# Kernel optimization log

Hardware: AMD Instinct MI355X
Metric: run time of the kernel (lower is better)

The kernel has to match this reference:

```python
import jax, jax.numpy as jnp
import numpy as np

N_NODES = 40000
N_EDGES = 400000
N_GRAPHS = 256
F_IN = 128
COND = 100
HEADS = 32
DIMS = [90, 45, 15, 5]
EPS = 1e-5


def setup_inputs() -> dict:
    key = jax.random.key(0)
    ks = iter(jax.random.split(key, 64))
    inp = {}
    inp["x"] = jax.random.normal(next(ks), (N_NODES, F_IN), dtype=jnp.float32)
    inp["edge_index"] = jax.random.randint(next(ks), (2, N_EDGES), 0, N_NODES, dtype=jnp.int32)
    inp["batch"] = jnp.sort(jax.random.randint(next(ks), (N_NODES,), 0, N_GRAPHS, dtype=jnp.int32))
    inp["conditional_features"] = jax.random.normal(next(ks), (COND,), dtype=jnp.float32)
    # GATConv params: W [in, H*C], a_src/a_dst [H, C], bias [C] (concat=False -> out is C)
    dims_in = [F_IN] + DIMS[:-1]
    for i, (ci, co) in enumerate(zip(dims_in, DIMS), start=1):
        sw = 1.0 / np.sqrt(ci)
        inp[f"W{i}"] = jax.random.normal(next(ks), (ci, HEADS * co), dtype=jnp.float32) * sw
        inp[f"as{i}"] = jax.random.normal(next(ks), (HEADS, co), dtype=jnp.float32) * (1.0 / np.sqrt(co))
        inp[f"ad{i}"] = jax.random.normal(next(ks), (HEADS, co), dtype=jnp.float32) * (1.0 / np.sqrt(co))
        inp[f"b{i}"] = jnp.zeros((co,), dtype=jnp.float32)
    # BatchNorm affine params (init gamma=1, beta=0) for sizes F_IN,90,45,15,5
    for i, c in enumerate([F_IN] + DIMS, start=1):
        inp[f"g{i}"] = jnp.ones((c,), dtype=jnp.float32)
        inp[f"be{i}"] = jnp.zeros((c,), dtype=jnp.float32)
    inp["fcW"] = jax.random.normal(next(ks), (DIMS[-1] + COND, 1), dtype=jnp.float32) * (1.0 / np.sqrt(DIMS[-1] + COND))
    inp["fcb"] = jnp.zeros((1,), dtype=jnp.float32)
    return inp


def _bn(x, g, b):
    # training-mode BatchNorm1d: batch statistics (biased var), eps=1e-5
    mu = x.mean(0)
    var = x.var(0)
    return g * (x - mu) * jax.lax.rsqrt(var + EPS) + b


def _gat(x, W, a_s, a_d, b, src, dst, n):
    H, C = a_s.shape
    h = (x @ W).reshape(n, H, C)                      # [N,H,C]
    s_src = jnp.einsum("nhc,hc->nh", h, a_s)
    s_dst = jnp.einsum("nhc,hc->nh", h, a_d)
    logit = jax.nn.leaky_relu(s_src[src] + s_dst[dst], 0.2)  # [E,H]
    m = jax.ops.segment_max(logit, dst, num_segments=n)
    e = jnp.exp(logit - m[dst])
    denom = jax.ops.segment_sum(e, dst, num_segments=n)
    alpha = e / denom[dst]                            # per-dst softmax, [E,H]
    out = jnp.zeros((n, C), dtype=x.dtype)
    for hi in range(H):  # fixed small loop over heads keeps peak memory at [E,C]
        out = out + jax.ops.segment_sum(alpha[:, hi, None] * h[src, hi, :], dst, num_segments=n)
    return out / H + b   # concat=False -> mean over heads, then bias


def reference(x, edge_index, batch, conditional_features,
              W1, as1, ad1, b1, W2, as2, ad2, b2, W3, as3, ad3, b3, W4, as4, ad4, b4,
              g1, be1, g2, be2, g3, be3, g4, be4, g5, be5, fcW, fcb):
    n = x.shape[0]
    loop = jnp.arange(n, dtype=edge_index.dtype)      # PyG GATConv adds self-loops by default
    src = jnp.concatenate([edge_index[0], loop])
    dst = jnp.concatenate([edge_index[1], loop])

    h = _bn(x, g1, be1)
    h = jax.nn.leaky_relu(_gat(h, W1, as1, ad1, b1, src, dst, n), 0.01)
    h = _bn(h, g2, be2)
    h = jax.nn.leaky_relu(_gat(h, W2, as2, ad2, b2, src, dst, n), 0.01)
    h = _bn(h, g3, be3)
    h = jax.nn.leaky_relu(_gat(h, W3, as3, ad3, b3, src, dst, n), 0.01)
    h = _bn(h, g4, be4)
    h = jax.nn.leaky_relu(_gat(h, W4, as4, ad4, b4, src, dst, n), 0.01)
    # dropout is identity in eval mode

    counts = jax.ops.segment_sum(jnp.ones((n,), dtype=h.dtype), batch, num_segments=N_GRAPHS)
    pooled = jax.ops.segment_sum(h, batch, num_segments=N_GRAPHS) / jnp.maximum(counts, 1.0)[:, None]
    z = jnp.concatenate([pooled, jnp.broadcast_to(conditional_features, (N_GRAPHS, COND))], axis=1)
    return jax.nn.sigmoid(z @ fcW + fcb).reshape(-1, 1)
```

## Files before the change

kernel.cpp:

```cpp
#include <hip/hip_runtime.h>
#include <hip/hip_bf16.h>

constexpr int NN = 40000;
constexpr int NE = 400000;
constexpr int NSLAB = 20000;
constexpr int MPAD = 20096;
constexpr int SCB = 256;
constexpr int SCHUNK = (NN + SCB - 1) / SCB;
constexpr int NPB = 512;

__device__ __forceinline__ unsigned short f2bf(float f) {
    unsigned int u = __float_as_uint(f);
    unsigned int r = (u + 0x7FFFu + ((u >> 16) & 1u)) >> 16;
    return (unsigned short)r;
}

__device__ __forceinline__ unsigned int cvt_pk_bf16(float a, float b) {
    unsigned int r;
    asm("v_cvt_pk_bf16_f32 %0, %1, %2" : "=v"(r) : "v"(a), "v"(b));
    return r;
}

__device__ __forceinline__ void load_lds16(const unsigned short* g, unsigned short* l) {
    __builtin_amdgcn_global_load_lds(
        (const __attribute__((address_space(1))) unsigned int*)(g),
        (__attribute__((address_space(3))) unsigned int*)(l), 16, 0, 0);
}

typedef __attribute__((ext_vector_type(8))) short bf16x8;
typedef __attribute__((ext_vector_type(4))) float f32x4;
typedef __attribute__((ext_vector_type(2))) float floatx2;

__global__ void bn_partial(const float* __restrict__ x, int N, int C,
                           float* __restrict__ partial) {
    int ch = threadIdx.x;
    if (ch >= C) return;
    float s = 0.f, sq = 0.f;
    for (int n = blockIdx.x; n < N; n += gridDim.x) {
        float v = x[(size_t)n * C + ch];
        s += v; sq += v * v;
    }
    partial[(size_t)blockIdx.x * 2 * C + ch]     = s;
    partial[(size_t)blockIdx.x * 2 * C + C + ch] = sq;
}

template <int CIN, int CP>
__global__ __launch_bounds__(256) void bn_apply_f(const float* __restrict__ x,
                                                  const float* __restrict__ partial,
                                                  const float* __restrict__ g,
                                                  const float* __restrict__ be,
                                                  float* __restrict__ scale_g,
                                                  float* __restrict__ shift_g,
                                                  unsigned short* __restrict__ xbn) {
    __shared__ float hs[2][128], hq[2][128];
    __shared__ float sc_l[CP], sh_l[CP];
    const int tid = threadIdx.x;
    const int half = tid >> 7, ch = tid & 127;
    if (ch < CIN) {
        float s = 0.f, sq = 0.f;
        for (int b = half * (NPB / 2); b < (half + 1) * (NPB / 2); ++b) {
            s  += partial[(size_t)b * 2 * CIN + ch];
            sq += partial[(size_t)b * 2 * CIN + CIN + ch];
        }
        hs[half][ch] = s; hq[half][ch] = sq;
    }
    __syncthreads();
    if (tid < CP) {
        float sc = 0.f, sh = 0.f;
        if (tid < CIN) {
            float s  = hs[0][tid] + hs[1][tid];
            float sq = hq[0][tid] + hq[1][tid];
            float mean = s / (float)NN;
            float var  = sq / (float)NN - mean * mean;
            float inv  = rsqrtf(var + 1e-5f);
            sc = g[tid] * inv;
            sh = be[tid] - mean * sc;
            if (blockIdx.x == 0) { scale_g[tid] = sc; shift_g[tid] = sh; }
        }
        sc_l[tid] = sc; sh_l[tid] = sh;
    }
    __syncthreads();
    const int total = NN * (CP / 2);
    for (int idx = blockIdx.x * 256 + tid; idx < total; idx += 256 * gridDim.x) {
        int n = idx / (CP / 2), c2 = idx % (CP / 2);
        int c = 2 * c2;
        float v0 = 0.f, v1 = 0.f;
        if (c < CIN)     v0 = sc_l[c] * x[(size_t)n * CIN + c] + sh_l[c];
        if (c + 1 < CIN) v1 = sc_l[c + 1] * x[(size_t)n * CIN + c + 1] + sh_l[c + 1];
        reinterpret_cast<unsigned int*>(xbn)[idx] = cvt_pk_bf16(v0, v1);
    }
}

struct PrepLayer {
    const float* W; const float* as_; const float* ad_;
    float* Wf; unsigned short* Wft; unsigned short* Wt;
    int CIN, CP, COUT, NP, bbase;
};
struct PrepArgs { PrepLayer L[4]; int nb; };

__global__ void prep_all(PrepArgs A) {
    int bid = blockIdx.x;
    int li = 0;
#pragma unroll
    for (int i = 1; i < 4; ++i)
        if (bid >= A.L[i].bbase) li = i;
    const PrepLayer& P = A.L[li];
    const int CIN = P.CIN, CP = P.CP, COUT = P.COUT;
    int b = bid - P.bbase;
    int tid = threadIdx.x;
    if (b < CP) {
        int cin = b;
        if (tid < 64) {
            int j = tid, h = j & 31;
            float s = 0.f;
            if (cin < CIN) {
                const float* a = (j < 32) ? P.as_ : P.ad_;
                const float* wrow = P.W + (size_t)cin * 32 * COUT + (size_t)h * COUT;
                const float* arow = a + (size_t)h * COUT;
                for (int c = 0; c < COUT; ++c) s += wrow[c] * arow[c];
            }
            P.Wf[cin * 64 + j] = s;
            P.Wft[j * CP + cin] = f2bf(s);
        }
    } else {
        int c = b - CP;
        for (int kk = tid; kk < 32 * CP; kk += blockDim.x) {
            int h = kk / CP, k = kk % CP;
            float v = 0.f;
            if (k < CIN && c < COUT)
                v = P.W[(size_t)k * (32 * COUT) + h * COUT + c] * (1.f / 32.f);
            P.Wt[(size_t)c * (32 * CP) + kk] = f2bf(v);
        }
    }
}

template <int CPK>
__global__ __launch_bounds__(256) void gemm_s(const unsigned short* __restrict__ xbn,
                                              const unsigned short* __restrict__ Wft,
                                              float* __restrict__ Sbuf) {
    constexpr int NC = CPK / 32;
    __shared__ unsigned short Ab[64 * 32];
    __shared__ unsigned short Bb[64 * 32];
    const int m0 = blockIdx.x * 64;
    const int tid = threadIdx.x;
    const int wv = tid >> 6, lane = tid & 63;
    const int mm = lane & 15, quad = lane >> 4;
    f32x4 acc[4];
#pragma unroll
    for (int t = 0; t < 4; ++t) acc[t] = f32x4{0.f, 0.f, 0.f, 0.f};

    for (int c = 0; c < NC; ++c) {
        int row = tid >> 2, gc = tid & 3;
        load_lds16(xbn + (size_t)(m0 + row) * CPK + c * 32 + gc * 8, Ab + (size_t)tid * 8);
        load_lds16(Wft + (size_t)row * CPK + c * 32 + gc * 8, Bb + (size_t)tid * 8);
        asm volatile("s_waitcnt vmcnt(0)" ::: "memory");
        __syncthreads();
        bf16x8 a = *reinterpret_cast<const bf16x8*>(&Ab[(wv * 16 + mm) * 32 + quad * 8]);
#pragma unroll
        for (int t = 0; t < 4; ++t) {
            bf16x8 b = *reinterpret_cast<const bf16x8*>(&Bb[(t * 16 + mm) * 32 + quad * 8]);
            acc[t] = __builtin_amdgcn_mfma_f32_16x16x32_bf16(a, b, acc[t], 0, 0, 0);
        }
        __syncthreads();
    }
    int rbase = m0 + wv * 16 + quad * 4;
#pragma unroll
    for (int t = 0; t < 4; ++t)
#pragma unroll
        for (int r = 0; r < 4; ++r)
            Sbuf[(size_t)(rbase + r) * 64 + t * 16 + mm] = acc[t][r];
}

__global__ __launch_bounds__(256) void gemm_bn(const float* __restrict__ X,
                                               const float* __restrict__ W,
                                               const float* __restrict__ scale,
                                               const float* __restrict__ shift,
                                               int Cin, int HC, float* __restrict__ OUT) {
    __shared__ float As[8][64];
    __shared__ float Bs[8][64];
    int tid = threadIdx.x;
    int n0 = blockIdx.y * 64;
    int j0 = blockIdx.x * 64;
    int tr = tid >> 4, tc = tid & 15;
    float acc[4][4] = {};
    for (int k0 = 0; k0 < Cin; k0 += 8) {
        int idx = tid;
#pragma unroll
        for (int it = 0; it < 2; ++it, idx += 256) {
            int row = idx >> 3, kk = idx & 7;
            int k = k0 + kk;
            float v = 0.f;
            if (k < Cin) v = scale[k] * X[(size_t)(n0 + row) * Cin + k] + shift[k];
            As[kk][row] = v;
        }
        int idx2 = tid;
#pragma unroll
        for (int it = 0; it < 2; ++it, idx2 += 256) {
            int col = idx2 & 63, kr = idx2 >> 6;
            int k = k0 + kr, j = j0 + col;
            float v = 0.f;
            if (k < Cin && j < HC) v = W[(size_t)k * HC + j];
            Bs[kr][col] = v;
        }
        __syncthreads();
#pragma unroll
        for (int kk = 0; kk < 8; ++kk) {
            float a[4], b[4];
#pragma unroll
            for (int i = 0; i < 4; ++i) a[i] = As[kk][tr * 4 + i];
#pragma unroll
            for (int j = 0; j < 4; ++j) b[j] = Bs[kk][tc * 4 + j];
#pragma unroll
            for (int i = 0; i < 4; ++i)
#pragma unroll
                for (int j = 0; j < 4; ++j) acc[i][j] += a[i] * b[j];
        }
        __syncthreads();
    }
#pragma unroll
    for (int i = 0; i < 4; ++i) {
        int row = n0 + tr * 4 + i;
#pragma unroll
        for (int j = 0; j < 4; ++j) {
            int col = j0 + tc * 4 + j;
            if (col < HC) OUT[(size_t)row * HC + col] = acc[i][j];
        }
    }
}

__global__ void count_kernel(const int* __restrict__ dst, int* __restrict__ deg) {
    int e = blockIdx.x * blockDim.x + threadIdx.x;
    if (e < NE) atomicAdd(&deg[dst[e]], 1);
}
__global__ void scan_pass1(const int* __restrict__ deg, int* __restrict__ bsum) {
    __shared__ int red[256];
    int b = blockIdx.x, t = threadIdx.x;
    int lo = b * SCHUNK, hi = min(lo + SCHUNK, NN);
    int s = 0;
    for (int i = lo + t; i < hi; i += 256) s += deg[i] + 1;
    red[t] = s;
    __syncthreads();
    for (int off = 128; off > 0; off >>= 1) {
        if (t < off) red[t] += red[t + off];
        __syncthreads();
    }
    if (t == 0) bsum[b] = red[0];
}
__global__ void scan_pass2(const int* __restrict__ bsum, int* __restrict__ boff,
                           int* __restrict__ rowptr) {
    __shared__ int lds[256];
    int t = threadIdx.x;
    int v0 = bsum[t];
    lds[t] = v0;
    __syncthreads();
    for (int off = 1; off < 256; off <<= 1) {
        int v = (t >= off) ? lds[t - off] : 0;
        __syncthreads();
        lds[t] += v;
        __syncthreads();
    }
    boff[t] = lds[t] - v0;
    if (t == 255) rowptr[NN] = lds[255];
}
__global__ void scan_pass3(const int* __restrict__ deg, const int* __restrict__ boff,
                           int* __restrict__ rowptr, int* __restrict__ cursor) {
    __shared__ int lds[256];
    int b = blockIdx.x, t = threadIdx.x;
    int i = b * SCHUNK + t;
    int d = (t < SCHUNK && i < NN) ? (deg[i] + 1) : 0;
    lds[t] = d;
    __syncthreads();
    for (int off = 1; off < 256; off <<= 1) {
        int v = (t >= off) ? lds[t - off] : 0;
        __syncthreads();
        lds[t] += v;
        __syncthreads();
    }
    if (t < SCHUNK && i < NN) {
        int excl = lds[t] - d + boff[b];
        rowptr[i] = excl;
        cursor[i] = excl;
    }
}
__global__ void scatter_all(const int* __restrict__ src, const int* __restrict__ dst,
                            int* __restrict__ cursor, int* __restrict__ colsrc) {
    int e = blockIdx.x * blockDim.x + threadIdx.x;
    if (e < NE) {
        int pos = atomicAdd(&cursor[dst[e]], 1);
        colsrc[pos] = src[e];
    } else if (e < NE + NN) {
        int n = e - NE;
        int pos = atomicAdd(&cursor[n], 1);
        colsrc[pos] = n;
    }
}

template <int CIN, int CP>
__global__ __launch_bounds__(256) void agg_x(const unsigned short* __restrict__ xbn,
                                             const float* __restrict__ S,
                                             const int* __restrict__ rowptr,
                                             const int* __restrict__ colsrc,
                                             int n0, unsigned short* __restrict__ z) {
    constexpr int BS = 256, CH = 16, J = CP / 8;
    constexpr bool V4 = (J % 4 == 0);
    constexpr int NACC = V4 ? (J / 4) : (J / 2);
    constexpr int LIT = CH * 32 / 256;
    __shared__ __align__(16) float x_lds[CH * CP];
    __shared__ float w_lds[CH * 32];
    __shared__ int cs_lds[CH];
    __shared__ float red_m[8][32];
    __shared__ float red_s[8][32];

    int n = n0 + blockIdx.x;
    int tid = threadIdx.x;
    int start = rowptr[n], end = rowptr[n + 1];
    const int h = tid & 31, g = tid >> 5;
    const int cbase = g * J;
    const float sd = S[(size_t)n * 64 + 32 + h];

    float m_reg = -INFINITY, d_reg = 0.f;
    f32x4 acc4[V4 ? NACC : 1];
    floatx2 acc2[V4 ? 1 : NACC];
    if constexpr (V4) {
#pragma unroll
        for (int j = 0; j < NACC; ++j) acc4[j] = f32x4{0.f, 0.f, 0.f, 0.f};
    } else {
#pragma unroll
        for (int j = 0; j < NACC; ++j) acc2[j] = floatx2{0.f, 0.f};
    }

    for (int chunk = start; chunk < end; chunk += CH) {
        int ce = min(CH, end - chunk);
        int ce32 = ce * 32;
        if (tid < CH && tid < ce) cs_lds[tid] = colsrc[chunk + tid];
        __syncthreads();

        float lreg[LIT];
        float pmx = -INFINITY;
#pragma unroll
        for (int p = 0; p < LIT; ++p) {
            int idx = p * 256 + tid;
            lreg[p] = -INFINITY;
            if (idx < ce32) {
                int e = idx >> 5;
                float l = S[(size_t)cs_lds[e] * 64 + h] + sd;
                l = l > 0.f ? l : 0.2f * l;
                lreg[p] = l;
                pmx = fmaxf(pmx, l);
            }
        }
        red_m[g][h] = pmx;
        for (int idx = tid; idx < ce * (CP / 4); idx += BS) {
            int e = idx / (CP / 4), c4 = idx % (CP / 4);
            uint2 u = reinterpret_cast<const uint2*>(xbn)[(size_t)cs_lds[e] * (CP / 4) + c4];
            f32x4 t;
            t[0] = __uint_as_float(u.x << 16);
            t[1] = __uint_as_float(u.x & 0xFFFF0000u);
            t[2] = __uint_as_float(u.y << 16);
            t[3] = __uint_as_float(u.y & 0xFFFF0000u);
            *reinterpret_cast<f32x4*>(&x_lds[e * CP + 4 * c4]) = t;
        }
        __syncthreads();

        float cm = red_m[0][h];
#pragma unroll
        for (int s2 = 1; s2 < 8; ++s2) cm = fmaxf(cm, red_m[s2][h]);
        float newm = fmaxf(m_reg, cm);
        float r = (m_reg == -INFINITY) ? 0.f : __expf(m_reg - newm);
        m_reg = newm;

        float ps = 0.f;
#pragma unroll
        for (int p = 0; p < LIT; ++p) {
            int idx = p * 256 + tid;
            if (idx < ce32) {
                float v = __expf(lreg[p] - m_reg);
                w_lds[idx] = v;
                ps += v;
            }
        }
        red_s[g][h] = ps;
        __syncthreads();

        float ss = red_s[0][h];
#pragma unroll
        for (int s2 = 1; s2 < 8; ++s2) ss += red_s[s2][h];
        d_reg = d_reg * r + ss;

        if constexpr (V4) {
            f32x4 rr4 = {r, r, r, r};
#pragma unroll
            for (int j = 0; j < NACC; ++j) acc4[j] *= rr4;
            for (int e = 0; e < ce; ++e) {
                float w = w_lds[e * 32 + h];
                f32x4 w4 = {w, w, w, w};
                const f32x4* xv = reinterpret_cast<const f32x4*>(&x_lds[e * CP + cbase]);
#pragma unroll
                for (int j = 0; j < NACC; ++j) acc4[j] += w4 * xv[j];
            }
        } else {
            floatx2 rr2 = {r, r};
#pragma unroll
            for (int j = 0; j < NACC; ++j) acc2[j] *= rr2;
            for (int e = 0; e < ce; ++e) {
                float w = w_lds[e * 32 + h];
                floatx2 w2 = {w, w};
                const floatx2* xv = reinterpret_cast<const floatx2*>(&x_lds[e * CP + cbase]);
#pragma unroll
                for (int j = 0; j < NACC; ++j) acc2[j] += w2 * xv[j];
            }
        }
    }

    float dinv = 1.f / d_reg;
    if constexpr (V4) {
        uint2* zp = reinterpret_cast<uint2*>(
            z + (size_t)(n - n0) * (32 * CP) + h * CP + cbase);
#pragma unroll
        for (int j = 0; j < NACC; ++j) {
            uint2 t;
            t.x = cvt_pk_bf16(acc4[j][0] * dinv, acc4[j][1] * dinv);
            t.y = cvt_pk_bf16(acc4[j][2] * dinv, acc4[j][3] * dinv);
            zp[j] = t;
        }
    } else {
        unsigned int* zp = reinterpret_cast<unsigned int*>(
            z + (size_t)(n - n0) * (32 * CP) + h * CP + cbase);
#pragma unroll
        for (int j = 0; j < NACC; ++j)
            zp[j] = cvt_pk_bf16(acc2[j][0] * dinv, acc2[j][1] * dinv);
    }
}

template <int NT, int KP, int KS, bool FB>
__global__ __launch_bounds__(256) void gemm_z_t(const unsigned short* __restrict__ z,
                                                const unsigned short* __restrict__ Wt,
                                                float* __restrict__ obuf,
                                                const float* __restrict__ bias,
                                                int n0, int COUT) {
    constexpr int NP = NT * 16;
    constexpr int KSEG = KP / KS;
    constexpr int NC = KSEG / 64;
    constexpr int MT = 64;
    __shared__ unsigned short Abuf[2][MT * 64];
    __shared__ unsigned short Bbuf[2][NP * 64];

    const int m0 = blockIdx.x * MT;
    const int kbeg = blockIdx.y * KSEG;
    const int tid = threadIdx.x;
    const int wv = tid >> 6;
    const int lane = tid & 63;
    const int mm = lane & 15, quad = lane >> 4;

    auto stage = [&](int buf, int kk) {
#pragma unroll
        for (int it = 0; it < 2; ++it) {
            int gi = it * 256 + tid;
            int row = gi >> 3, gc = gi & 7;
            int srow = m0 + row;
            if (srow > NSLAB - 1) srow = NSLAB - 1;
            const unsigned short* src = z + (size_t)srow * KP + kk + gc * 8;
            unsigned short* dst = &Abuf[buf][(size_t)(it * 256 + wv * 64) * 8];
            load_lds16(src, dst);
        }
#pragma unroll
        for (int it = 0; it < (NP * 8 + 255) / 256; ++it) {
            int gi = it * 256 + tid;
            if (gi < NP * 8) {
                int row = gi >> 3, gc = gi & 7;
                const unsigned short* src = Wt + (size_t)row * KP + kk + gc * 8;
                unsigned short* dst = &Bbuf[buf][(size_t)(it * 256 + wv * 64) * 8];
                load_lds16(src, dst);
            }
        }
    };

    f32x4 acc[NT];
#pragma unroll
    for (int t = 0; t < NT; ++t) acc[t] = f32x4{0.f, 0.f, 0.f, 0.f};

    stage(0, kbeg);
    for (int c = 0; c < NC; ++c) {
        asm volatile("s_waitcnt vmcnt(0)" ::: "memory");
        __syncthreads();
        int cur = c & 1;
        if (c + 1 < NC) stage(cur ^ 1, kbeg + (c + 1) * 64);
        const unsigned short* Ab = Abuf[cur];
        const unsigned short* Bb = Bbuf[cur];
#pragma unroll
        for (int hh = 0; hh < 2; ++hh) {
            bf16x8 a0 = *reinterpret_cast<const bf16x8*>(&Ab[(wv * 16 + mm) * 64 + hh * 32 + quad * 8]);
#pragma unroll
            for (int t = 0; t < NT; ++t) {
                bf16x8 b = *reinterpret_cast<const bf16x8*>(&Bb[(t * 16 + mm) * 64 + hh * 32 + quad * 8]);
                acc[t] = __builtin_amdgcn_mfma_f32_16x16x32_bf16(a0, b, acc[t], 0, 0, 0);
            }
        }
        __syncthreads();
    }

    int row0 = quad * 4;
    if constexpr (FB) {
#pragma unroll
        for (int t = 0; t < NT; ++t) {
            int cc = t * 16 + mm;
#pragma unroll
            for (int r = 0; r < 4; ++r) {
                int m = m0 + wv * 16 + row0 + r;
                if (m < NSLAB && cc < COUT) {
                    float v = acc[t][r] + bias[cc];
                    v = v > 0.f ? v : 0.01f * v;
                    obuf[(size_t)(n0 + m) * COUT + cc] = v;
                }
            }
        }
    } else {
        float* pb = obuf + (size_t)blockIdx.y * MPAD * NP;
#pragma unroll
        for (int t = 0; t < NT; ++t) {
            int cc = t * 16 + mm;
#pragma unroll
            for (int r = 0; r < 4; ++r) {
                int m = m0 + wv * 16 + row0 + r;
                pb[(size_t)m * NP + cc] = acc[t][r];
            }
        }
    }
}

__global__ void reduce_parts(const float* __restrict__ pbuf, int KS, int NPAD, int COUT,
                             const float* __restrict__ bias, int n0,
                             float* __restrict__ xout) {
    int idx = blockIdx.x * blockDim.x + threadIdx.x;
    if (idx >= NSLAB * NPAD) return;
    int m = idx / NPAD, c = idx % NPAD;
    if (c >= COUT) return;
    float s = 0.f;
    for (int p = 0; p < KS; ++p) s += pbuf[(size_t)p * MPAD * NPAD + (size_t)m * NPAD + c];
    float v = s + bias[c];
    v = v > 0.f ? v : 0.01f * v;
    xout[(size_t)(n0 + m) * COUT + c] = v;
}

__global__ __launch_bounds__(64) void pool_head(const float* __restrict__ x4,
                                                const int* __restrict__ batch,
                                                const float* __restrict__ cond,
                                                const float* __restrict__ fcW,
                                                const float* __restrict__ fcb,
                                                float* __restrict__ out) {
    int g = blockIdx.x;
    int lane = threadIdx.x;
    int lo = 0, hi = NN;
    while (lo < hi) { int mid = (lo + hi) >> 1; if (batch[mid] < g) lo = mid + 1; else hi = mid; }
    int lo2 = lo, hi2 = NN;
    while (lo2 < hi2) { int mid = (lo2 + hi2) >> 1; if (batch[mid] < g + 1) lo2 = mid + 1; else hi2 = mid; }
    int beg = lo, end = lo2;

    float s[5] = {0.f, 0.f, 0.f, 0.f, 0.f};
    for (int n = beg + lane; n < end; n += 64) {
#pragma unroll
        for (int c = 0; c < 5; ++c) s[c] += x4[(size_t)n * 5 + c];
    }
    float cz = 0.f;
    if (lane < 100) cz = cond[lane] * fcW[5 + lane];
    if (lane + 64 < 100) cz += cond[lane + 64] * fcW[5 + lane + 64];
#pragma unroll
    for (int off = 32; off > 0; off >>= 1) {
#pragma unroll
        for (int c = 0; c < 5; ++c) s[c] += __shfl_down(s[c], off, 64);
        cz += __shfl_down(cz, off, 64);
    }
    if (lane == 0) {
        float cnt = fmaxf((float)(end - beg), 1.f);
        float zv = fcb[0] + cz;
#pragma unroll
        for (int c = 0; c < 5; ++c) zv += (s[c] / cnt) * fcW[c];
        out[g] = 1.f / (1.f + __expf(-zv));
    }
}

struct LayerBufs {
    float* partial; float* scale; float* shift;
    unsigned short* xbn; unsigned short* zbuf;
    float* Sbuf; float* pbuf; const int* rowptr; const int* colsrc;
};

template <int CIN, int CP, int COUT, int NP, int NT, int KS>
static void run_layer(const float* xin, const float* Wf, const unsigned short* Wft,
                      const unsigned short* Wt,
                      const float* Bv, const float* G, const float* Be,
                      float* xout, const LayerBufs& B, hipStream_t stream) {
    constexpr int KP = 32 * CP;
    constexpr int NPAD = NT * 16;
    bn_partial<<<NPB, 128, 0, stream>>>(xin, NN, CIN, B.partial);
    bn_apply_f<CIN, CP><<<512, 256, 0, stream>>>(xin, B.partial, G, Be,
                                                 B.scale, B.shift, B.xbn);
    if constexpr (CP >= 64) {
        gemm_s<CP><<<NN / 64, 256, 0, stream>>>(B.xbn, Wft, B.Sbuf);
    } else {
        gemm_bn<<<dim3(1, NN / 64), 256, 0, stream>>>(xin, Wf, B.scale, B.shift, CIN, 64, B.Sbuf);
    }
    for (int s = 0; s < 2; ++s) {
        int n0 = s * NSLAB;
        agg_x<CIN, CP><<<NSLAB, 256, 0, stream>>>(B.xbn, B.Sbuf, B.rowptr, B.colsrc, n0, B.zbuf);
        if constexpr (KS > 1) {
            gemm_z_t<NT, KP, KS, false><<<dim3(MPAD / 64, KS), 256, 0, stream>>>(
                B.zbuf, Wt, B.pbuf, nullptr, n0, COUT);
            reduce_parts<<<(NSLAB * NPAD + 255) / 256, 256, 0, stream>>>(
                B.pbuf, KS, NPAD, COUT, Bv, n0, xout);
        } else {
            gemm_z_t<NT, KP, 1, true><<<dim3(MPAD / 64, 1), 256, 0, stream>>>(
                B.zbuf, Wt, xout, Bv, n0, COUT);
        }
    }
}

extern "C" void kernel_launch(void* const* d_in, const int* in_sizes, int n_in,
                              void* d_out, int out_size, void* d_ws, size_t ws_size,
                              hipStream_t stream) {
    (void)in_sizes; (void)n_in; (void)out_size;
    const float* x     = (const float*)d_in[0];
    const int*   ei    = (const int*)d_in[1];
    const int*   batch = (const int*)d_in[2];
    const float* cond  = (const float*)d_in[3];
    const float* W[4]  = {(const float*)d_in[4],  (const float*)d_in[8],
                          (const float*)d_in[12], (const float*)d_in[16]};
    const float* Asp[4] = {(const float*)d_in[5],  (const float*)d_in[9],
                           (const float*)d_in[13], (const float*)d_in[17]};
    const float* Adp[4] = {(const float*)d_in[6],  (const float*)d_in[10],
                           (const float*)d_in[14], (const float*)d_in[18]};
    const float* Bv[4]  = {(const float*)d_in[7],  (const float*)d_in[11],
                           (const float*)d_in[15], (const float*)d_in[19]};
    const float* G[4]   = {(const float*)d_in[20], (const float*)d_in[22],
                           (const float*)d_in[24], (const float*)d_in[26]};
    const float* Be[4]  = {(const float*)d_in[21], (const float*)d_in[23],
                           (const float*)d_in[25], (const float*)d_in[27]};
    const float* fcW = (const float*)d_in[30];
    const float* fcb = (const float*)d_in[31];
    float* out = (float*)d_out;

    char* base = (char*)d_ws;
    size_t off = 0;
    auto alloc = [&](size_t b) {
        size_t o = off;
        off += (b + 255) & ~(size_t)255;
        return (void*)(base + o);
    };
    unsigned short* zbuf = (unsigned short*)alloc((size_t)NSLAB * 4096 * 2);
    unsigned short* xbn  = (unsigned short*)alloc((size_t)NN * 128 * 2);
    float* pbuf    = (float*)alloc((size_t)4 * MPAD * 96 * 4);
    float* xbuf    = (float*)alloc((size_t)NN * 90 * 4);
    float* Sbuf    = (float*)alloc((size_t)NN * 64 * 4);
    float* partial = (float*)alloc((size_t)NPB * 2 * 128 * 4);
    float* scale   = (float*)alloc(128 * 4);
    float* shift   = (float*)alloc(128 * 4);
    const int CPs[4]  = {128, 96, 48, 16};
    const int NPs[4]  = {96, 48, 16, 16};
    const int CINs[4] = {128, 90, 45, 15};
    const int COUTs[4] = {90, 45, 15, 5};
    float* Wf_a[4]; unsigned short* Wft_a[4]; unsigned short* Wt_a[4];
    for (int i = 0; i < 4; ++i) {
        Wf_a[i]  = (float*)alloc((size_t)CPs[i] * 64 * 4);
        Wft_a[i] = (unsigned short*)alloc((size_t)64 * CPs[i] * 2);
        Wt_a[i]  = (unsigned short*)alloc((size_t)NPs[i] * 32 * CPs[i] * 2);
    }
    int* deg     = (int*)alloc((size_t)NN * 4);
    int* rowptr  = (int*)alloc((size_t)(NN + 1) * 4);
    int* cursor  = (int*)alloc((size_t)NN * 4);
    int* colsrc  = (int*)alloc((size_t)(NE + NN) * 4);
    int* bsum    = (int*)alloc((size_t)SCB * 4);
    int* boff    = (int*)alloc((size_t)SCB * 4);
    if (off > ws_size) return;

    const int* srcp = ei;
    const int* dstp = ei + NE;

    PrepArgs PA;
    int bb = 0;
    for (int i = 0; i < 4; ++i) {
        PA.L[i] = PrepLayer{W[i], Asp[i], Adp[i], Wf_a[i], Wft_a[i], Wt_a[i],
                            CINs[i], CPs[i], COUTs[i], NPs[i], bb};
        bb += CPs[i] + NPs[i];
    }
    PA.nb = bb;
    prep_all<<<bb, 256, 0, stream>>>(PA);

    hipMemsetAsync(deg, 0, (size_t)NN * 4, stream);
    count_kernel<<<(NE + 255) / 256, 256, 0, stream>>>(dstp, deg);
    scan_pass1<<<SCB, 256, 0, stream>>>(deg, bsum);
    scan_pass2<<<1, 256, 0, stream>>>(bsum, boff, rowptr);
    scan_pass3<<<SCB, 256, 0, stream>>>(deg, boff, rowptr, cursor);
    scatter_all<<<(NE + NN + 255) / 256, 256, 0, stream>>>(srcp, dstp, cursor, colsrc);

    LayerBufs B{partial, scale, shift, xbn, zbuf, Sbuf, pbuf, rowptr, colsrc};

    run_layer<128, 128, 90, 96, 6, 4>(x,    Wf_a[0], Wft_a[0], Wt_a[0], Bv[0], G[0], Be[0], xbuf, B, stream);
    run_layer< 90,  96, 45, 48, 3, 3>(xbuf, Wf_a[1], Wft_a[1], Wt_a[1], Bv[1], G[1], Be[1], xbuf, B, stream);
    run_layer< 45,  48, 15, 16, 1, 1>(xbuf, Wf_a[2], Wft_a[2], Wt_a[2], Bv[2], G[2], Be[2], xbuf, B, stream);
    run_layer< 15,  16,  5, 16, 1, 1>(xbuf, Wf_a[3], Wft_a[3], Wt_a[3], Bv[3], G[3], Be[3], xbuf, B, stream);

    pool_head<<<256, 64, 0, stream>>>(xbuf, batch, cond, fcW, fcb, out);
}
```

Baseline: 1.018 ms.

## Process two destination nodes per block in GAT aggregation kernel

The aggregation kernel now handles two nodes per 256-thread block, with 128 threads per node and each thread group covering twice as many channels. LDS buffers are duplicated per node, and the grid is halved. The aim is to raise work per thread and amortize block overhead and barriers. In exchange, both nodes loop to the larger degree, so work is imbalanced, and the code assumes CP/4 is a multiple of 4, dropping the float2 path.

```diff
diff --git a/kernel.cpp b/kernel.cpp
--- a/kernel.cpp
+++ b/kernel.cpp
@@ -29,7 +29,6 @@
 
 typedef __attribute__((ext_vector_type(8))) short bf16x8;
 typedef __attribute__((ext_vector_type(4))) float f32x4;
-typedef __attribute__((ext_vector_type(2))) float floatx2;
 
 __global__ void bn_partial(const float* __restrict__ x, int N, int C,
                            float* __restrict__ partial) {
@@ -301,70 +300,74 @@
                                              const int* __restrict__ rowptr,
                                              const int* __restrict__ colsrc,
                                              int n0, unsigned short* __restrict__ z) {
-    constexpr int BS = 256, CH = 16, J = CP / 8;
-    constexpr bool V4 = (J % 4 == 0);
-    constexpr int NACC = V4 ? (J / 4) : (J / 2);
-    constexpr int LIT = CH * 32 / 256;
-    __shared__ __align__(16) float x_lds[CH * CP];
-    __shared__ float w_lds[CH * 32];
-    __shared__ int cs_lds[CH];
-    __shared__ float red_m[8][32];
-    __shared__ float red_s[8][32];
-
-    int n = n0 + blockIdx.x;
-    int tid = threadIdx.x;
-    int start = rowptr[n], end = rowptr[n + 1];
-    const int h = tid & 31, g = tid >> 5;
+    constexpr int CH = 16, J = CP / 4;
+    constexpr int NACC = J / 4;
+    constexpr int LIT = CH * 32 / 128;
+    __shared__ __align__(16) float x_lds[2][CH * CP];
+    __shared__ float w_lds[2][CH * 32];
+    __shared__ int cs_lds[2][CH];
+    __shared__ float red_m[2][4][32];
+    __shared__ float red_s[2][4][32];
+
+    const int tid = threadIdx.x;
+    const int node = tid >> 7;
+    const int tl = tid & 127;
+    const int h = tl & 31, g = tl >> 5;
     const int cbase = g * J;
+    const int nb = n0 + blockIdx.x * 2;
+    const int n = nb + node;
+
+    const int r0 = rowptr[nb], r1 = rowptr[nb + 1], r2 = rowptr[nb + 2];
+    const int start = node ? r1 : r0;
+    const int end   = node ? r2 : r1;
+    const int nch = (max(r1 - r0, r2 - r1) + CH - 1) / CH;
+
     const float sd = S[(size_t)n * 64 + 32 + h];
 
     float m_reg = -INFINITY, d_reg = 0.f;
-    f32x4 acc4[V4 ? NACC : 1];
-    floatx2 acc2[V4 ? 1 : NACC];
-    if constexpr (V4) {
-#pragma unroll
-        for (int j = 0; j < NACC; ++j) acc4[j] = f32x4{0.f, 0.f, 0.f, 0.f};
-    } else {
-#pragma unroll
-        for (int j = 0; j < NACC; ++j) acc2[j] = floatx2{0.f, 0.f};
-    }
-
-    for (int chunk = start; chunk < end; chunk += CH) {
+    f32x4 acc4[NACC];
+#pragma unroll
+    for (int j = 0; j < NACC; ++j) acc4[j] = f32x4{0.f, 0.f, 0.f, 0.f};
+
+    for (int t = 0; t < nch; ++t) {
+        int chunk = start + t * CH;
         int ce = min(CH, end - chunk);
+        if (ce < 0) ce = 0;
         int ce32 = ce * 32;
-        if (tid < CH && tid < ce) cs_lds[tid] = colsrc[chunk + tid];
+        if (tl < CH && tl < ce) cs_lds[node][tl] = colsrc[chunk + tl];
         __syncthreads();
 
         float lreg[LIT];
         float pmx = -INFINITY;
 #pragma unroll
         for (int p = 0; p < LIT; ++p) {
-            int idx = p * 256 + tid;
+            int idx = p * 128 + tl;
             lreg[p] = -INFINITY;
             if (idx < ce32) {
                 int e = idx >> 5;
-                float l = S[(size_t)cs_lds[e] * 64 + h] + sd;
+                float l = S[(size_t)cs_lds[node][e] * 64 + h] + sd;
                 l = l > 0.f ? l : 0.2f * l;
                 lreg[p] = l;
                 pmx = fmaxf(pmx, l);
             }
         }
-        red_m[g][h] = pmx;
-        for (int idx = tid; idx < ce * (CP / 4); idx += BS) {
+        red_m[node][g][h] = pmx;
+        for (int idx = tl; idx < ce * (CP / 4); idx += 128) {
             int e = idx / (CP / 4), c4 = idx % (CP / 4);
-            uint2 u = reinterpret_cast<const uint2*>(xbn)[(size_t)cs_lds[e] * (CP / 4) + c4];
-            f32x4 t;
-            t[0] = __uint_as_float(u.x << 16);
-            t[1] = __uint_as_float(u.x & 0xFFFF0000u);
-            t[2] = __uint_as_float(u.y << 16);
-            t[3] = __uint_as_float(u.y & 0xFFFF0000u);
-            *reinterpret_cast<f32x4*>(&x_lds[e * CP + 4 * c4]) = t;
-        }
-        __syncthreads();
-
-        float cm = red_m[0][h];
-#pragma unroll
-        for (int s2 = 1; s2 < 8; ++s2) cm = fmaxf(cm, red_m[s2][h]);
+            uint2 u = reinterpret_cast<const uint2*>(xbn)
+                          [(size_t)cs_lds[node][e] * (CP / 4) + c4];
+            f32x4 tt;
+            tt[0] = __uint_as_float(u.x << 16);
+            tt[1] = __uint_as_float(u.x & 0xFFFF0000u);
+            tt[2] = __uint_as_float(u.y << 16);
+            tt[3] = __uint_as_float(u.y & 0xFFFF0000u);
+            *reinterpret_cast<f32x4*>(&x_lds[node][e * CP + 4 * c4]) = tt;
+        }
+        __syncthreads();
+
+        float cm = red_m[node][0][h];
+#pragma unroll
+        for (int s2 = 1; s2 < 4; ++s2) cm = fmaxf(cm, red_m[node][s2][h]);
         float newm = fmaxf(m_reg, cm);
         float r = (m_reg == -INFINITY) ? 0.f : __expf(m_reg - newm);
         m_reg = newm;
@@ -372,63 +375,42 @@
         float ps = 0.f;
 #pragma unroll
         for (int p = 0; p < LIT; ++p) {
-            int idx = p * 256 + tid;
+            int idx = p * 128 + tl;
             if (idx < ce32) {
                 float v = __expf(lreg[p] - m_reg);
-                w_lds[idx] = v;
+                w_lds[node][idx] = v;
                 ps += v;
             }
         }
-        red_s[g][h] = ps;
-        __syncthreads();
-
-        float ss = red_s[0][h];
-#pragma unroll
-        for (int s2 = 1; s2 < 8; ++s2) ss += red_s[s2][h];
+        red_s[node][g][h] = ps;
+        __syncthreads();
+
+        float ss = red_s[node][0][h];
+#pragma unroll
+        for (int s2 = 1; s2 < 4; ++s2) ss += red_s[node][s2][h];
         d_reg = d_reg * r + ss;
 
-        if constexpr (V4) {
-            f32x4 rr4 = {r, r, r, r};
-#pragma unroll
-            for (int j = 0; j < NACC; ++j) acc4[j] *= rr4;
-            for (int e = 0; e < ce; ++e) {
-                float w = w_lds[e * 32 + h];
-                f32x4 w4 = {w, w, w, w};
-                const f32x4* xv = reinterpret_cast<const f32x4*>(&x_lds[e * CP + cbase]);
-#pragma unroll
-                for (int j = 0; j < NACC; ++j) acc4[j] += w4 * xv[j];
-            }
-        } else {
-            floatx2 rr2 = {r, r};
-#pragma unroll
-            for (int j = 0; j < NACC; ++j) acc2[j] *= rr2;
-            for (int e = 0; e < ce; ++e) {
-                float w = w_lds[e * 32 + h];
-                floatx2 w2 = {w, w};
-                const floatx2* xv = reinterpret_cast<const floatx2*>(&x_lds[e * CP + cbase]);
-#pragma unroll
-                for (int j = 0; j < NACC; ++j) acc2[j] += w2 * xv[j];
-            }
+        f32x4 rr4 = {r, r, r, r};
+#pragma unroll
+        for (int j = 0; j < NACC; ++j) acc4[j] *= rr4;
+        for (int e = 0; e < ce; ++e) {
+            float w = w_lds[node][e * 32 + h];
+            f32x4 w4 = {w, w, w, w};
+            const f32x4* xv = reinterpret_cast<const f32x4*>(&x_lds[node][e * CP + cbase]);
+#pragma unroll
+            for (int j = 0; j < NACC; ++j) acc4[j] += w4 * xv[j];
         }
     }
 
     float dinv = 1.f / d_reg;
-    if constexpr (V4) {
-        uint2* zp = reinterpret_cast<uint2*>(
-            z + (size_t)(n - n0) * (32 * CP) + h * CP + cbase);
-#pragma unroll
-        for (int j = 0; j < NACC; ++j) {
-            uint2 t;
-            t.x = cvt_pk_bf16(acc4[j][0] * dinv, acc4[j][1] * dinv);
-            t.y = cvt_pk_bf16(acc4[j][2] * dinv, acc4[j][3] * dinv);
-            zp[j] = t;
-        }
-    } else {
-        unsigned int* zp = reinterpret_cast<unsigned int*>(
-            z + (size_t)(n - n0) * (32 * CP) + h * CP + cbase);
-#pragma unroll
-        for (int j = 0; j < NACC; ++j)
-            zp[j] = cvt_pk_bf16(acc2[j][0] * dinv, acc2[j][1] * dinv);
+    uint2* zp = reinterpret_cast<uint2*>(
+        z + (size_t)(n - n0) * (32 * CP) + h * CP + cbase);
+#pragma unroll
+    for (int j = 0; j < NACC; ++j) {
+        uint2 tt;
+        tt.x = cvt_pk_bf16(acc4[j][0] * dinv, acc4[j][1] * dinv);
+        tt.y = cvt_pk_bf16(acc4[j][2] * dinv, acc4[j][3] * dinv);
+        zp[j] = tt;
     }
 }
 
@@ -602,7 +584,7 @@
     }
     for (int s = 0; s < 2; ++s) {
         int n0 = s * NSLAB;
-        agg_x<CIN, CP><<<NSLAB, 256, 0, stream>>>(B.xbn, B.Sbuf, B.rowptr, B.colsrc, n0, B.zbuf);
+        agg_x<CIN, CP><<<NSLAB / 2, 256, 0, stream>>>(B.xbn, B.Sbuf, B.rowptr, B.colsrc, n0, B.zbuf);
         if constexpr (KS > 1) {
             gemm_z_t<NT, KP, KS, false><<<dim3(MPAD / 64, KS), 256, 0, stream>>>(
                 B.zbuf, Wt, B.pbuf, nullptr, n0, COUT);
```

Result: slower. 1.047 ms (+2.9%).

## Fuse BatchNorm statistics into GEMM epilogues and process small layers in one slab

Applied to the files above, without the earlier changes.

Computes the per-channel sum and sum-of-squares for the next BatchNorm inside the producing kernels: the K-split reduce kernel and the fused-bias GEMM epilogue. This removes the separate bn_partial pass over the activations for layers 2-4. Layers 3 and 4 now run as a single slab over all nodes instead of two, which halves their launches. The cost is extra reductions and shared-memory traffic in the epilogues, and partial-count bookkeeping that must match the grid sizes used.

```diff
diff --git a/kernel.cpp b/kernel.cpp
--- a/kernel.cpp
+++ b/kernel.cpp
@@ -47,6 +47,7 @@
 template <int CIN, int CP>
 __global__ __launch_bounds__(256) void bn_apply_f(const float* __restrict__ x,
                                                   const float* __restrict__ partial,
+                                                  int nb,
                                                   const float* __restrict__ g,
                                                   const float* __restrict__ be,
                                                   float* __restrict__ scale_g,
@@ -57,8 +58,10 @@
     const int tid = threadIdx.x;
     const int half = tid >> 7, ch = tid & 127;
     if (ch < CIN) {
+        int b0 = half ? (nb >> 1) : 0;
+        int b1 = half ? nb : (nb >> 1);
         float s = 0.f, sq = 0.f;
-        for (int b = half * (NPB / 2); b < (half + 1) * (NPB / 2); ++b) {
+        for (int b = b0; b < b1; ++b) {
             s  += partial[(size_t)b * 2 * CIN + ch];
             sq += partial[(size_t)b * 2 * CIN + CIN + ch];
         }
@@ -432,12 +435,13 @@
     }
 }
 
-template <int NT, int KP, int KS, bool FB>
+template <int NT, int KP, int KS, bool FB, bool STATS>
 __global__ __launch_bounds__(256) void gemm_z_t(const unsigned short* __restrict__ z,
                                                 const unsigned short* __restrict__ Wt,
                                                 float* __restrict__ obuf,
                                                 const float* __restrict__ bias,
-                                                int n0, int COUT) {
+                                                int n0, int COUT, int nr,
+                                                float* __restrict__ statp) {
     constexpr int NP = NT * 16;
     constexpr int KSEG = KP / KS;
     constexpr int NC = KSEG / 64;
@@ -458,7 +462,7 @@
             int gi = it * 256 + tid;
             int row = gi >> 3, gc = gi & 7;
             int srow = m0 + row;
-            if (srow > NSLAB - 1) srow = NSLAB - 1;
+            if (srow > nr - 1) srow = nr - 1;
             const unsigned short* src = z + (size_t)srow * KP + kk + gc * 8;
             unsigned short* dst = &Abuf[buf][(size_t)(it * 256 + wv * 64) * 8];
             load_lds16(src, dst);
@@ -501,16 +505,37 @@
 
     int row0 = quad * 4;
     if constexpr (FB) {
+        float s = 0.f, q = 0.f;
 #pragma unroll
         for (int t = 0; t < NT; ++t) {
             int cc = t * 16 + mm;
 #pragma unroll
             for (int r = 0; r < 4; ++r) {
                 int m = m0 + wv * 16 + row0 + r;
-                if (m < NSLAB && cc < COUT) {
+                if (m < nr && cc < COUT) {
                     float v = acc[t][r] + bias[cc];
                     v = v > 0.f ? v : 0.01f * v;
                     obuf[(size_t)(n0 + m) * COUT + cc] = v;
+                    if constexpr (STATS) { s += v; q += v * v; }
+                }
+            }
+        }
+        if constexpr (STATS) {
+            static_assert(NT == 1, "STATS path assumes NT==1");
+            __shared__ float ssum[4][4][16], sqsum[4][4][16];
+            ssum[wv][quad][mm] = s; sqsum[wv][quad][mm] = q;
+            __syncthreads();
+            if (tid < 16) {
+                float S = 0.f, Q = 0.f;
+#pragma unroll
+                for (int a = 0; a < 4; ++a)
+#pragma unroll
+                    for (int b2 = 0; b2 < 4; ++b2) {
+                        S += ssum[a][b2][tid]; Q += sqsum[a][b2][tid];
+                    }
+                if (tid < COUT) {
+                    statp[(size_t)blockIdx.x * 2 * COUT + tid] = S;
+                    statp[(size_t)blockIdx.x * 2 * COUT + COUT + tid] = Q;
                 }
             }
         }
@@ -528,18 +553,30 @@
     }
 }
 
-__global__ void reduce_parts(const float* __restrict__ pbuf, int KS, int NPAD, int COUT,
-                             const float* __restrict__ bias, int n0,
-                             float* __restrict__ xout) {
-    int idx = blockIdx.x * blockDim.x + threadIdx.x;
-    if (idx >= NSLAB * NPAD) return;
-    int m = idx / NPAD, c = idx % NPAD;
-    if (c >= COUT) return;
-    float s = 0.f;
-    for (int p = 0; p < KS; ++p) s += pbuf[(size_t)p * MPAD * NPAD + (size_t)m * NPAD + c];
-    float v = s + bias[c];
-    v = v > 0.f ? v : 0.01f * v;
-    xout[(size_t)(n0 + m) * COUT + c] = v;
+template <int NPAD>
+__global__ void reduce_parts_stats(const float* __restrict__ pbuf, int KS, int COUT,
+                                   const float* __restrict__ bias, int n0, int slab,
+                                   float* __restrict__ xout, float* __restrict__ statp) {
+    const int c = threadIdx.x;
+    const bool act = (c < COUT);
+    const float bv = act ? bias[c] : 0.f;
+    float s = 0.f, q = 0.f;
+    for (int m = blockIdx.x; m < NSLAB; m += gridDim.x) {
+        float t = 0.f;
+        for (int p = 0; p < KS; ++p)
+            t += pbuf[(size_t)p * MPAD * NPAD + (size_t)m * NPAD + c];
+        if (act) {
+            float v = t + bv;
+            v = v > 0.f ? v : 0.01f * v;
+            xout[(size_t)(n0 + m) * COUT + c] = v;
+            s += v; q += v * v;
+        }
+    }
+    if (act) {
+        int b = slab * gridDim.x + blockIdx.x;
+        statp[(size_t)b * 2 * COUT + c] = s;
+        statp[(size_t)b * 2 * COUT + COUT + c] = q;
+    }
 }
 
 __global__ __launch_bounds__(64) void pool_head(const float* __restrict__ x4,
@@ -580,37 +617,39 @@
 }
 
 struct LayerBufs {
-    float* partial; float* scale; float* shift;
+    float* scale; float* shift;
     unsigned short* xbn; unsigned short* zbuf;
     float* Sbuf; float* pbuf; const int* rowptr; const int* colsrc;
 };
 
-template <int CIN, int CP, int COUT, int NP, int NT, int KS>
-static void run_layer(const float* xin, const float* Wf, const unsigned short* Wft,
+template <int CIN, int CP, int COUT, int NP, int NT, int KS, int SLABS, bool OSTATS>
+static void run_layer(const float* xin, const float* sp_in, int nb_in,
+                      const float* Wf, const unsigned short* Wft,
                       const unsigned short* Wt,
                       const float* Bv, const float* G, const float* Be,
-                      float* xout, const LayerBufs& B, hipStream_t stream) {
+                      float* xout, float* statp, const LayerBufs& B, hipStream_t stream) {
     constexpr int KP = 32 * CP;
     constexpr int NPAD = NT * 16;
-    bn_partial<<<NPB, 128, 0, stream>>>(xin, NN, CIN, B.partial);
-    bn_apply_f<CIN, CP><<<512, 256, 0, stream>>>(xin, B.partial, G, Be,
+    constexpr int NR = NN / SLABS;
+    bn_apply_f<CIN, CP><<<512, 256, 0, stream>>>(xin, sp_in, nb_in, G, Be,
                                                  B.scale, B.shift, B.xbn);
     if constexpr (CP >= 64) {
         gemm_s<CP><<<NN / 64, 256, 0, stream>>>(B.xbn, Wft, B.Sbuf);
     } else {
         gemm_bn<<<dim3(1, NN / 64), 256, 0, stream>>>(xin, Wf, B.scale, B.shift, CIN, 64, B.Sbuf);
     }
-    for (int s = 0; s < 2; ++s) {
-        int n0 = s * NSLAB;
-        agg_x<CIN, CP><<<NSLAB, 256, 0, stream>>>(B.xbn, B.Sbuf, B.rowptr, B.colsrc, n0, B.zbuf);
+    for (int s = 0; s < SLABS; ++s) {
+        int n0 = s * NR;
+        agg_x<CIN, CP><<<NR, 256, 0, stream>>>(B.xbn, B.Sbuf, B.rowptr, B.colsrc, n0, B.zbuf);
         if constexpr (KS > 1) {
-            gemm_z_t<NT, KP, KS, false><<<dim3(MPAD / 64, KS), 256, 0, stream>>>(
-                B.zbuf, Wt, B.pbuf, nullptr, n0, COUT);
-            reduce_parts<<<(NSLAB * NPAD + 255) / 256, 256, 0, stream>>>(
-                B.pbuf, KS, NPAD, COUT, Bv, n0, xout);
+            static_assert(SLABS == 2, "K-split path assumes NSLAB rows");
+            gemm_z_t<NT, KP, KS, false, false><<<dim3(MPAD / 64, KS), 256, 0, stream>>>(
+                B.zbuf, Wt, B.pbuf, nullptr, n0, COUT, NR, nullptr);
+            reduce_parts_stats<NPAD><<<256, NPAD, 0, stream>>>(
+                B.pbuf, KS, COUT, Bv, n0, s, xout, statp);
         } else {
-            gemm_z_t<NT, KP, 1, true><<<dim3(MPAD / 64, 1), 256, 0, stream>>>(
-                B.zbuf, Wt, xout, Bv, n0, COUT);
+            gemm_z_t<NT, KP, 1, true, OSTATS><<<dim3((NR + 63) / 64, 1), 256, 0, stream>>>(
+                B.zbuf, Wt, xout, Bv, n0, COUT, NR, statp);
         }
     }
 }
@@ -652,6 +691,7 @@
     float* xbuf    = (float*)alloc((size_t)NN * 90 * 4);
     float* Sbuf    = (float*)alloc((size_t)NN * 64 * 4);
     float* partial = (float*)alloc((size_t)NPB * 2 * 128 * 4);
+    float* stat1   = (float*)alloc((size_t)NPB * 2 * 128 * 4);
     float* scale   = (float*)alloc(128 * 4);
     float* shift   = (float*)alloc(128 * 4);
     const int CPs[4]  = {128, 96, 48, 16};
@@ -692,12 +732,18 @@
     scan_pass3<<<SCB, 256, 0, stream>>>(deg, boff, rowptr, cursor);
     scatter_all<<<(NE + NN + 255) / 256, 256, 0, stream>>>(srcp, dstp, cursor, colsrc);
 
-    LayerBufs B{partial, scale, shift, xbn, zbuf, Sbuf, pbuf, rowptr, colsrc};
-
-    run_layer<128, 128, 90, 96, 6, 4>(x,    Wf_a[0], Wft_a[0], Wt_a[0], Bv[0], G[0], Be[0], xbuf, B, stream);
-    run_layer< 90,  96, 45, 48, 3, 3>(xbuf, Wf_a[1], Wft_a[1], Wt_a[1], Bv[1], G[1], Be[1], xbuf, B, stream);
-    run_layer< 45,  48, 15, 16, 1, 1>(xbuf, Wf_a[2], Wft_a[2], Wt_a[2], Bv[2], G[2], Be[2], xbuf, B, stream);
-    run_layer< 15,  16,  5, 16, 1, 1>(xbuf, Wf_a[3], Wft_a[3], Wt_a[3], Bv[3], G[3], Be[3], xbuf, B, stream);
+    LayerBufs B{scale, shift, xbn, zbuf, Sbuf, pbuf, rowptr, colsrc};
+
+    bn_partial<<<NPB, 128, 0, stream>>>(x, NN, 128, partial);
+
+    run_layer<128, 128, 90, 96, 6, 4, 2, false>(x, partial, NPB,
+        Wf_a[0], Wft_a[0], Wt_a[0], Bv[0], G[0], Be[0], xbuf, stat1, B, stream);
+    run_layer< 90,  96, 45, 48, 3, 3, 2, false>(xbuf, stat1, 512,
+        Wf_a[1], Wft_a[1], Wt_a[1], Bv[1], G[1], Be[1], xbuf, partial, B, stream);
+    run_layer< 45,  48, 15, 16, 1, 1, 1, true >(xbuf, partial, 512,
+        Wf_a[2], Wft_a[2], Wt_a[2], Bv[2], G[2], Be[2], xbuf, stat1, B, stream);
+    run_layer< 15,  16,  5, 16, 1, 1, 1, false>(xbuf, stat1, 625,
+        Wf_a[3], Wft_a[3], Wt_a[3], Bv[3], G[3], Be[3], xbuf, stat1, B, stream);
 
     pool_head<<<256, 64, 0, stream>>>(xbuf, batch, cond, fcW, fcb, out);
 }
```

Result: slower. 1.442 ms (+41.7%).
